# Optimization experiments

Hardware: AMD Instinct MI355X
Metric: run time of the kernel (lower is better)

The kernel has to match this reference:

```python
import jax, jax.numpy as jnp
import numpy as np

EMBED_DIM = 1024
SCALE = float(np.sqrt(EMBED_DIM))


def setup_inputs() -> dict:
    key = jax.random.key(0)
    ks = jax.random.split(key, 4)
    B, S, D = 4, 2048, EMBED_DIM
    x = jax.random.normal(ks[0], (B, S, D), dtype=jnp.float32)
    # causal mask: 1 where attention allowed, 0 where blocked
    mask = jnp.tril(jnp.ones((S, S), dtype=jnp.int32))
    init = 1.0 / np.sqrt(D)
    Wq = jax.random.normal(ks[1], (D, D), dtype=jnp.float32) * init
    Wk = jax.random.normal(ks[2], (D, D), dtype=jnp.float32) * init
    Wv = jax.random.normal(ks[3], (D, D), dtype=jnp.float32) * init
    bq = jnp.zeros((D,), dtype=jnp.float32)
    bk = jnp.zeros((D,), dtype=jnp.float32)
    bv = jnp.zeros((D,), dtype=jnp.float32)
    return {"x": x, "mask": mask, "Wq": Wq, "bq": bq, "Wk": Wk, "bk": bk, "Wv": Wv, "bv": bv}


def reference(x, mask, Wq, bq, Wk, bk, Wv, bv):
    # Q, K, V projections (torch Linear: x @ W^T + b; here W stored as (D_in, D_out))
    q = x @ Wq + bq  # (B, S, D)
    k = x @ Wk + bk
    v = x @ Wv + bv
    # attention scores: Q K^T / sqrt(D)
    scores = jnp.einsum("bsd,btd->bst", q, k) / SCALE  # (B, S, S)
    scores = jnp.where(mask == 0, -jnp.inf, scores)
    attn = jax.nn.softmax(scores, axis=-1)
    # dropout disabled (inference / eval mode)
    out = jnp.einsum("bst,btd->bsd", attn, v)  # (B, S, D)
    return out
```

## Files before the change

### kernel.cpp

```cpp
#include <hip/hip_runtime.h>
#include <math.h>

#define DMODEL 1024
#define SEQ 2048
#define BATCH 4
#define SCALE_INV (1.0f/32.0f)

typedef unsigned short ushort_t;
typedef __attribute__((ext_vector_type(8))) short bf16x8;
typedef __attribute__((ext_vector_type(4))) float f32x4;

__device__ __forceinline__ ushort_t f2bf(float f) {
    unsigned int u = __float_as_uint(f);
    unsigned int rounding = 0x7FFFu + ((u >> 16) & 1u);
    return (ushort_t)((u + rounding) >> 16);
}

#define GLOAD16(SRC, DST) \
    __builtin_amdgcn_global_load_lds( \
        (const __attribute__((address_space(1))) void*)(SRC), \
        (__attribute__((address_space(3))) void*)(DST), 16, 0, 0)

__device__ __forceinline__ int xcd_swz(int bid, int nwg) {
    return (bid & 7) * (nwg >> 3) + (bid >> 3);
}

__device__ __forceinline__ void gemm_core_128(
    const ushort_t* __restrict__ A, int lda,
    const ushort_t* __restrict__ Bt, int ldb,
    int arow0, int brow0, int ksteps,
    ushort_t* As, ushort_t* Bs,
    f32x4 acc[4][4])
{
    const int tid = threadIdx.x;
    const int l   = tid & 63;
    const int w   = tid >> 6;
    const int wr  = w >> 1;
    const int wc  = w & 1;
    const int ke_swz = (((l & 3) ^ ((l >> 2) & 3)) * 8);
    const int kgx = (l >> 4) ^ (l & 3);

    for (int s = 0; s < ksteps; ++s) {
        const int k0 = s * 32;
        #pragma unroll
        for (int i = 0; i < 2; ++i) {
            const int off = i * 4096 + w * 1024 + l * 16;
            const int row = off >> 6;
            GLOAD16(A + (size_t)(arow0 + row) * lda + k0 + ke_swz,
                    (char*)As + i * 4096 + w * 1024);
        }
        #pragma unroll
        for (int i = 0; i < 2; ++i) {
            const int off = i * 4096 + w * 1024 + l * 16;
            const int row = off >> 6;
            GLOAD16(Bt + (size_t)(brow0 + row) * ldb + k0 + ke_swz,
                    (char*)Bs + i * 4096 + w * 1024);
        }
        __syncthreads();

        bf16x8 a[4], b[4];
        #pragma unroll
        for (int m = 0; m < 4; ++m)
            a[m] = *(const bf16x8*)(As + (wr * 64 + m * 16 + (l & 15)) * 32 + kgx * 8);
        #pragma unroll
        for (int n = 0; n < 4; ++n)
            b[n] = *(const bf16x8*)(Bs + (wc * 64 + n * 16 + (l & 15)) * 32 + kgx * 8);
        #pragma unroll
        for (int m = 0; m < 4; ++m)
            #pragma unroll
            for (int n = 0; n < 4; ++n)
                acc[m][n] = __builtin_amdgcn_mfma_f32_16x16x32_bf16(a[m], b[n], acc[m][n], 0, 0, 0);
        __syncthreads();
    }
}

__global__ __launch_bounds__(256) void qkv_gemm_mfma(
    const ushort_t* __restrict__ x,
    const ushort_t* __restrict__ wtq, const ushort_t* __restrict__ wtk, const ushort_t* __restrict__ wtv,
    const float* __restrict__ bq, const float* __restrict__ bk, const float* __restrict__ bv,
    ushort_t* __restrict__ q, ushort_t* __restrict__ k, ushort_t* __restrict__ vt)
{
    __shared__ __align__(16) ushort_t As[128 * 32];
    __shared__ __align__(16) ushort_t Bs[128 * 32];

    const int wg = xcd_swz(blockIdx.x, 8 * 64 * 3);
    const int z  = wg >> 9;
    const int r  = wg & 511;
    const int by = r >> 3;
    const int bx = r & 7;

    const ushort_t* Bt; const float* bias; float scale;
    if (z == 0)      { Bt = wtq; bias = bq; scale = SCALE_INV; }
    else if (z == 1) { Bt = wtk; bias = bk; scale = 1.0f; }
    else             { Bt = wtv; bias = bv; scale = 1.0f; }

    const int arow0 = by * 128;
    const int brow0 = bx * 128;

    f32x4 acc[4][4];
    #pragma unroll
    for (int m = 0; m < 4; ++m)
        #pragma unroll
        for (int n = 0; n < 4; ++n)
            acc[m][n] = (f32x4)(0.f);

    gemm_core_128(x, DMODEL, Bt, DMODEL, arow0, brow0, DMODEL / 32, As, Bs, acc);

    const int l  = threadIdx.x & 63;
    const int w  = threadIdx.x >> 6;
    const int wr = w >> 1, wc = w & 1;

    if (z < 2) {
        ushort_t* out = (z == 0) ? q : k;
        #pragma unroll
        for (int n = 0; n < 4; ++n) {
            const int gcol = brow0 + wc * 64 + n * 16 + (l & 15);
            const float bb = bias[gcol];
            #pragma unroll
            for (int m = 0; m < 4; ++m) {
                #pragma unroll
                for (int j = 0; j < 4; ++j) {
                    const int grow = arow0 + wr * 64 + m * 16 + (l >> 4) * 4 + j;
                    out[(size_t)grow * DMODEL + gcol] = f2bf((acc[m][n][j] + bb) * scale);
                }
            }
        }
    } else {
        ushort_t* vtb = vt + (size_t)(arow0 >> 11) * DMODEL * SEQ;
        #pragma unroll
        for (int n = 0; n < 4; ++n) {
            const int gcol = brow0 + wc * 64 + n * 16 + (l & 15);
            const float bb = bias[gcol];
            #pragma unroll
            for (int m = 0; m < 4; ++m) {
                const int t0 = (arow0 & 2047) + wr * 64 + m * 16 + (l >> 4) * 4;
                ushort4 o;
                o.x = f2bf(acc[m][n][0] + bb);
                o.y = f2bf(acc[m][n][1] + bb);
                o.z = f2bf(acc[m][n][2] + bb);
                o.w = f2bf(acc[m][n][3] + bb);
                *(ushort4*)(vtb + (size_t)gcol * SEQ + t0) = o;
            }
        }
    }
}

__global__ __launch_bounds__(256) void qkt_gemm_mfma(
    const ushort_t* __restrict__ q, const ushort_t* __restrict__ k,
    float* __restrict__ scores)
{
    const int wg = xcd_swz(blockIdx.x, 16 * 16 * BATCH);
    const int b  = wg >> 8;
    const int r  = wg & 255;
    const int st = r >> 4;
    const int tt = r & 15;
    if (tt > st) return;

    __shared__ __align__(16) ushort_t As[128 * 32];
    __shared__ __align__(16) ushort_t Bs[128 * 32];

    const ushort_t* A  = q + (size_t)b * SEQ * DMODEL;
    const ushort_t* Bt = k + (size_t)b * SEQ * DMODEL;
    float* out = scores + (size_t)b * SEQ * SEQ;

    f32x4 acc[4][4];
    #pragma unroll
    for (int m = 0; m < 4; ++m)
        #pragma unroll
        for (int n = 0; n < 4; ++n)
            acc[m][n] = (f32x4)(0.f);

    gemm_core_128(A, DMODEL, Bt, DMODEL, st * 128, tt * 128, DMODEL / 32, As, Bs, acc);

    const int l  = threadIdx.x & 63;
    const int w  = threadIdx.x >> 6;
    const int wr = w >> 1, wc = w & 1;
    #pragma unroll
    for (int m = 0; m < 4; ++m) {
        #pragma unroll
        for (int n = 0; n < 4; ++n) {
            const int gcol = tt * 128 + wc * 64 + n * 16 + (l & 15);
            #pragma unroll
            for (int j = 0; j < 4; ++j) {
                const int grow = st * 128 + wr * 64 + m * 16 + (l >> 4) * 4 + j;
                out[(size_t)grow * SEQ + gcol] = acc[m][n][j];
            }
        }
    }
}

__global__ __launch_bounds__(256) void softmax_rows(float* __restrict__ scores)
{
    const int s = blockIdx.x;
    const int b = blockIdx.y;
    const int tid = threadIdx.x;

    float* row = scores + ((size_t)b * SEQ + s) * SEQ;
    ushort_t* prow = (ushort_t*)row;
    const int nt = s + 1;

    __shared__ float e_sh[SEQ];
    __shared__ float red[256];

    float lmax = -INFINITY;
    const int nt4 = nt >> 2;
    for (int i = tid; i < nt4; i += 256) {
        const float4 f = ((const float4*)row)[i];
        ((float4*)e_sh)[i] = f;
        lmax = fmaxf(lmax, fmaxf(fmaxf(f.x, f.y), fmaxf(f.z, f.w)));
    }
    for (int t = nt4 * 4 + tid; t < nt; t += 256) {
        const float xv = row[t];
        e_sh[t] = xv;
        lmax = fmaxf(lmax, xv);
    }
    red[tid] = lmax;
    __syncthreads();
    for (int off = 128; off > 0; off >>= 1) {
        if (tid < off) red[tid] = fmaxf(red[tid], red[tid + off]);
        __syncthreads();
    }
    const float mx = red[0];
    __syncthreads();

    float lsum = 0.f;
    for (int t = tid; t < nt; t += 256) {
        const float e = __expf(e_sh[t] - mx);
        e_sh[t] = e;
        lsum += e;
    }
    red[tid] = lsum;
    __syncthreads();
    for (int off = 128; off > 0; off >>= 1) {
        if (tid < off) red[tid] += red[tid + off];
        __syncthreads();
    }
    const float inv = 1.0f / red[0];
    __syncthreads();

    const int tmax = ((s >> 7) + 1) << 7;
    for (int t4 = tid * 4; t4 < tmax; t4 += 1024) {
        ushort4 o;
        o.x = (t4     < nt) ? f2bf(e_sh[t4    ] * inv) : (ushort_t)0;
        o.y = (t4 + 1 < nt) ? f2bf(e_sh[t4 + 1] * inv) : (ushort_t)0;
        o.z = (t4 + 2 < nt) ? f2bf(e_sh[t4 + 2] * inv) : (ushort_t)0;
        o.w = (t4 + 3 < nt) ? f2bf(e_sh[t4 + 3] * inv) : (ushort_t)0;
        *(ushort4*)(prow + t4) = o;
    }
}

__global__ __launch_bounds__(256) void pv_gemm_mfma(
    const float* __restrict__ scoresP, const ushort_t* __restrict__ vt,
    float* __restrict__ outp)
{
    const int wg = xcd_swz(blockIdx.x, 8 * 16 * BATCH);
    const int b  = wg >> 7;
    const int r  = wg & 127;
    const int st = r >> 3;
    const int dt = r & 7;

    __shared__ __align__(16) ushort_t As[128 * 32];
    __shared__ __align__(16) ushort_t Bs[128 * 32];

    const ushort_t* A  = (const ushort_t*)(scoresP + (size_t)b * SEQ * SEQ);
    const ushort_t* Bt = vt + (size_t)b * DMODEL * SEQ;
    float* out = outp + (size_t)b * SEQ * DMODEL;

    f32x4 acc[4][4];
    #pragma unroll
    for (int m = 0; m < 4; ++m)
        #pragma unroll
        for (int n = 0; n < 4; ++n)
            acc[m][n] = (f32x4)(0.f);

    const int ksteps = (st + 1) * 4;
    gemm_core_128(A, 2 * SEQ, Bt, SEQ, st * 128, dt * 128, ksteps, As, Bs, acc);

    const int l  = threadIdx.x & 63;
    const int w  = threadIdx.x >> 6;
    const int wr = w >> 1, wc = w & 1;
    #pragma unroll
    for (int m = 0; m < 4; ++m) {
        #pragma unroll
        for (int n = 0; n < 4; ++n) {
            const int gcol = dt * 128 + wc * 64 + n * 16 + (l & 15);
            #pragma unroll
            for (int j = 0; j < 4; ++j) {
                const int grow = st * 128 + wr * 64 + m * 16 + (l >> 4) * 4 + j;
                out[(size_t)grow * DMODEL + gcol] = acc[m][n][j];
            }
        }
    }
}

__global__ __launch_bounds__(256) void convert_bf16(
    const float* __restrict__ in, ushort_t* __restrict__ out, int n4)
{
    const int i = (blockIdx.x * 256 + threadIdx.x);
    if (i < n4) {
        const float4 f = *(const float4*)(in + (size_t)i * 4);
        ushort4 o;
        o.x = f2bf(f.x); o.y = f2bf(f.y); o.z = f2bf(f.z); o.w = f2bf(f.w);
        *(ushort4*)(out + (size_t)i * 4) = o;
    }
}

__global__ __launch_bounds__(256) void transpose_w(
    const float* __restrict__ Wq, const float* __restrict__ Wk, const float* __restrict__ Wv,
    ushort_t* __restrict__ wtq, ushort_t* __restrict__ wtk, ushort_t* __restrict__ wtv)
{
    const float* W; ushort_t* wt;
    const int z = blockIdx.z;
    if (z == 0)      { W = Wq; wt = wtq; }
    else if (z == 1) { W = Wk; wt = wtk; }
    else             { W = Wv; wt = wtv; }

    __shared__ float tile[32][33];
    const int k0 = blockIdx.x * 32, n0 = blockIdx.y * 32;
    const int x = threadIdx.x, y = threadIdx.y;
    #pragma unroll
    for (int i = 0; i < 4; ++i)
        tile[y + i * 8][x] = W[(size_t)(k0 + y + i * 8) * DMODEL + n0 + x];
    __syncthreads();
    #pragma unroll
    for (int i = 0; i < 4; ++i)
        wt[(size_t)(n0 + y + i * 8) * DMODEL + k0 + x] = f2bf(tile[x][y + i * 8]);
}

__global__ __launch_bounds__(1024) void qkv_gemm_f32(
    const float* __restrict__ x,
    const float* __restrict__ Wq, const float* __restrict__ bq,
    const float* __restrict__ Wk, const float* __restrict__ bk,
    const float* __restrict__ Wv, const float* __restrict__ bv,
    float* __restrict__ q, float* __restrict__ k, float* __restrict__ v)
{
    const float* W; const float* bias; float* out;
    const int z = blockIdx.z;
    if (z == 0)      { W = Wq; bias = bq; out = q; }
    else if (z == 1) { W = Wk; bias = bk; out = k; }
    else             { W = Wv; bias = bv; out = v; }

    __shared__ float As[32][33];
    __shared__ float Bs[32][33];
    const int tx = threadIdx.x, ty = threadIdx.y;
    const int row = blockIdx.y * 32 + ty;
    const int col = blockIdx.x * 32 + tx;

    float acc = 0.f;
    for (int k0 = 0; k0 < DMODEL; k0 += 32) {
        As[ty][tx] = x[(size_t)row * DMODEL + k0 + tx];
        Bs[ty][tx] = W[(size_t)(k0 + ty) * DMODEL + col];
        __syncthreads();
        #pragma unroll
        for (int kk = 0; kk < 32; ++kk)
            acc += As[ty][kk] * Bs[kk][tx];
        __syncthreads();
    }
    out[(size_t)row * DMODEL + col] = acc + bias[col];
}

__global__ __launch_bounds__(256) void attn_f32(
    const float* __restrict__ q, const float* __restrict__ k,
    const float* __restrict__ v, float* __restrict__ out)
{
    const int s = blockIdx.x, b = blockIdx.y, tid = threadIdx.x;
    __shared__ float qs[DMODEL];
    __shared__ float sc[SEQ];
    __shared__ float red[256];
    const float* qrow = q + ((size_t)b * SEQ + s) * DMODEL;
    for (int d = tid; d < DMODEL; d += 256) qs[d] = qrow[d];
    __syncthreads();
    const float* kb = k + (size_t)b * SEQ * DMODEL;
    const int nt = s + 1;
    float lmax = -INFINITY;
    for (int t = tid; t < nt; t += 256) {
        const float* krow = kb + (size_t)t * DMODEL;
        float acc = 0.f;
        for (int d = 0; d < DMODEL; d += 4) {
            const float4 kv = *(const float4*)(krow + d);
            acc += qs[d] * kv.x + qs[d+1] * kv.y + qs[d+2] * kv.z + qs[d+3] * kv.w;
        }
        acc *= SCALE_INV; sc[t] = acc; lmax = fmaxf(lmax, acc);
    }
    red[tid] = lmax; __syncthreads();
    for (int off = 128; off > 0; off >>= 1) { if (tid < off) red[tid] = fmaxf(red[tid], red[tid+off]); __syncthreads(); }
    const float mx = red[0]; __syncthreads();
    float lsum = 0.f;
    for (int t = tid; t < nt; t += 256) { const float e = expf(sc[t]-mx); sc[t]=e; lsum+=e; }
    red[tid] = lsum; __syncthreads();
    for (int off = 128; off > 0; off >>= 1) { if (tid < off) red[tid] += red[tid+off]; __syncthreads(); }
    const float inv = 1.0f / red[0]; __syncthreads();
    const float* vb = v + (size_t)b * SEQ * DMODEL;
    float a0=0,a1=0,a2=0,a3=0;
    for (int t = 0; t < nt; ++t) {
        const float p = sc[t];
        const float* vrow = vb + (size_t)t * DMODEL;
        a0 += p*vrow[tid]; a1 += p*vrow[tid+256]; a2 += p*vrow[tid+512]; a3 += p*vrow[tid+768];
    }
    float* orow = out + ((size_t)b * SEQ + s) * DMODEL;
    orow[tid]=a0*inv; orow[tid+256]=a1*inv; orow[tid+512]=a2*inv; orow[tid+768]=a3*inv;
}

extern "C" void kernel_launch(void* const* d_in, const int* in_sizes, int n_in,
                              void* d_out, int out_size, void* d_ws, size_t ws_size,
                              hipStream_t stream)
{
    const float* x  = (const float*)d_in[0];
    const float* Wq = (const float*)d_in[2];
    const float* bq = (const float*)d_in[3];
    const float* Wk = (const float*)d_in[4];
    const float* bk = (const float*)d_in[5];
    const float* Wv = (const float*)d_in[6];
    const float* bv = (const float*)d_in[7];
    float* out = (float*)d_out;

    const size_t SZ_XBF   = (size_t)BATCH * SEQ * DMODEL * 2;
    const size_t SZ_WT    = (size_t)DMODEL * DMODEL * 2;
    const size_t SZ_QKV   = (size_t)BATCH * SEQ * DMODEL * 2;
    const size_t SZ_SC    = (size_t)BATCH * SEQ * SEQ * 4;
    const size_t NEED = SZ_XBF + 3 * SZ_WT + 3 * SZ_QKV + SZ_SC;

    if (ws_size >= NEED) {
        char* p = (char*)d_ws;
        ushort_t* x_bf = (ushort_t*)p;              p += SZ_XBF;
        ushort_t* wtq  = (ushort_t*)p;              p += SZ_WT;
        ushort_t* wtk  = (ushort_t*)p;              p += SZ_WT;
        ushort_t* wtv  = (ushort_t*)p;              p += SZ_WT;
        ushort_t* q_bf = (ushort_t*)p;              p += SZ_QKV;
        ushort_t* k_bf = (ushort_t*)p;              p += SZ_QKV;
        ushort_t* vt   = (ushort_t*)p;              p += SZ_QKV;
        float*    sc   = (float*)p;

        const int n4 = BATCH * SEQ * DMODEL / 4;
        hipLaunchKernelGGL(convert_bf16, dim3((n4 + 255) / 256), dim3(256), 0, stream,
                           x, x_bf, n4);
        hipLaunchKernelGGL(transpose_w, dim3(32, 32, 3), dim3(32, 8), 0, stream,
                           Wq, Wk, Wv, wtq, wtk, wtv);
        hipLaunchKernelGGL(qkv_gemm_mfma, dim3(8 * 64 * 3), dim3(256), 0, stream,
                           x_bf, wtq, wtk, wtv, bq, bk, bv, q_bf, k_bf, vt);
        hipLaunchKernelGGL(qkt_gemm_mfma, dim3(16 * 16 * BATCH), dim3(256), 0, stream,
                           q_bf, k_bf, sc);
        hipLaunchKernelGGL(softmax_rows, dim3(SEQ, BATCH), dim3(256), 0, stream, sc);
        hipLaunchKernelGGL(pv_gemm_mfma, dim3(8 * 16 * BATCH), dim3(256), 0, stream,
                           sc, vt, out);
    } else {
        const size_t elems = (size_t)BATCH * SEQ * DMODEL;
        float* q = (float*)d_ws;
        float* k = q + elems;
        float* v = k + elems;
        hipLaunchKernelGGL(qkv_gemm_f32, dim3(DMODEL / 32, BATCH * SEQ / 32, 3), dim3(32, 32), 0, stream,
                           x, Wq, bq, Wk, bk, Wv, bv, q, k, v);
        hipLaunchKernelGGL(attn_f32, dim3(SEQ, BATCH), dim3(256), 0, stream, q, k, v, out);
    }
}
```

Measured before the change: 206.7 us.

## Merge prep kernels, drop LDS swizzle, widen softmax to 512 threads

Merges the x-to-bf16 conversion and the weight transpose into one prep launch writing a contiguous weight buffer, and simplifies QKV weight selection to pointer arithmetic. Removes the XOR swizzle from the shared GEMM core's LDS load and read addressing, which may bring back LDS bank conflicts. Doubles softmax block size to 512 and vectorises the exp pass with float4. These combine launch-overhead, addressing and softmax parallelism changes with a possible bank-conflict regression.

After: 213.4 us. 3.2% more time.

```diff
diff --git a/kernel.cpp b/kernel.cpp
--- a/kernel.cpp
+++ b/kernel.cpp
@@ -37,8 +37,6 @@
     const int w   = tid >> 6;
     const int wr  = w >> 1;
     const int wc  = w & 1;
-    const int ke_swz = (((l & 3) ^ ((l >> 2) & 3)) * 8);
-    const int kgx = (l >> 4) ^ (l & 3);
 
     for (int s = 0; s < ksteps; ++s) {
         const int k0 = s * 32;
@@ -46,14 +44,16 @@
         for (int i = 0; i < 2; ++i) {
             const int off = i * 4096 + w * 1024 + l * 16;
             const int row = off >> 6;
-            GLOAD16(A + (size_t)(arow0 + row) * lda + k0 + ke_swz,
+            const int ke  = (off & 63) >> 1;
+            GLOAD16(A + (size_t)(arow0 + row) * lda + k0 + ke,
                     (char*)As + i * 4096 + w * 1024);
         }
         #pragma unroll
         for (int i = 0; i < 2; ++i) {
             const int off = i * 4096 + w * 1024 + l * 16;
             const int row = off >> 6;
-            GLOAD16(Bt + (size_t)(brow0 + row) * ldb + k0 + ke_swz,
+            const int ke  = (off & 63) >> 1;
+            GLOAD16(Bt + (size_t)(brow0 + row) * ldb + k0 + ke,
                     (char*)Bs + i * 4096 + w * 1024);
         }
         __syncthreads();
@@ -61,10 +61,10 @@
         bf16x8 a[4], b[4];
         #pragma unroll
         for (int m = 0; m < 4; ++m)
-            a[m] = *(const bf16x8*)(As + (wr * 64 + m * 16 + (l & 15)) * 32 + kgx * 8);
+            a[m] = *(const bf16x8*)(As + (wr * 64 + m * 16 + (l & 15)) * 32 + (l >> 4) * 8);
         #pragma unroll
         for (int n = 0; n < 4; ++n)
-            b[n] = *(const bf16x8*)(Bs + (wc * 64 + n * 16 + (l & 15)) * 32 + kgx * 8);
+            b[n] = *(const bf16x8*)(Bs + (wc * 64 + n * 16 + (l & 15)) * 32 + (l >> 4) * 8);
         #pragma unroll
         for (int m = 0; m < 4; ++m)
             #pragma unroll
@@ -76,7 +76,7 @@
 
 __global__ __launch_bounds__(256) void qkv_gemm_mfma(
     const ushort_t* __restrict__ x,
-    const ushort_t* __restrict__ wtq, const ushort_t* __restrict__ wtk, const ushort_t* __restrict__ wtv,
+    const ushort_t* __restrict__ wt,
     const float* __restrict__ bq, const float* __restrict__ bk, const float* __restrict__ bv,
     ushort_t* __restrict__ q, ushort_t* __restrict__ k, ushort_t* __restrict__ vt)
 {
@@ -89,10 +89,9 @@
     const int by = r >> 3;
     const int bx = r & 7;
 
-    const ushort_t* Bt; const float* bias; float scale;
-    if (z == 0)      { Bt = wtq; bias = bq; scale = SCALE_INV; }
-    else if (z == 1) { Bt = wtk; bias = bk; scale = 1.0f; }
-    else             { Bt = wtv; bias = bv; scale = 1.0f; }
+    const ushort_t* Bt = wt + (size_t)z * DMODEL * DMODEL;
+    const float* bias = (z == 0) ? bq : (z == 1) ? bk : bv;
+    const float scale = (z == 0) ? SCALE_INV : 1.0f;
 
     const int arow0 = by * 128;
     const int brow0 = bx * 128;
@@ -189,7 +188,7 @@
     }
 }
 
-__global__ __launch_bounds__(256) void softmax_rows(float* __restrict__ scores)
+__global__ __launch_bounds__(512) void softmax_rows(float* __restrict__ scores)
 {
     const int s = blockIdx.x;
     const int b = blockIdx.y;
@@ -200,23 +199,23 @@
     const int nt = s + 1;
 
     __shared__ float e_sh[SEQ];
-    __shared__ float red[256];
+    __shared__ float red[512];
 
     float lmax = -INFINITY;
     const int nt4 = nt >> 2;
-    for (int i = tid; i < nt4; i += 256) {
+    for (int i = tid; i < nt4; i += 512) {
         const float4 f = ((const float4*)row)[i];
         ((float4*)e_sh)[i] = f;
         lmax = fmaxf(lmax, fmaxf(fmaxf(f.x, f.y), fmaxf(f.z, f.w)));
     }
-    for (int t = nt4 * 4 + tid; t < nt; t += 256) {
+    for (int t = nt4 * 4 + tid; t < nt; t += 512) {
         const float xv = row[t];
         e_sh[t] = xv;
         lmax = fmaxf(lmax, xv);
     }
     red[tid] = lmax;
     __syncthreads();
-    for (int off = 128; off > 0; off >>= 1) {
+    for (int off = 256; off > 0; off >>= 1) {
         if (tid < off) red[tid] = fmaxf(red[tid], red[tid + off]);
         __syncthreads();
     }
@@ -224,14 +223,21 @@
     __syncthreads();
 
     float lsum = 0.f;
-    for (int t = tid; t < nt; t += 256) {
+    for (int i = tid; i < nt4; i += 512) {
+        float4 f = ((const float4*)e_sh)[i];
+        f.x = __expf(f.x - mx); f.y = __expf(f.y - mx);
+        f.z = __expf(f.z - mx); f.w = __expf(f.w - mx);
+        ((float4*)e_sh)[i] = f;
+        lsum += f.x + f.y + f.z + f.w;
+    }
+    for (int t = nt4 * 4 + tid; t < nt; t += 512) {
         const float e = __expf(e_sh[t] - mx);
         e_sh[t] = e;
         lsum += e;
     }
     red[tid] = lsum;
     __syncthreads();
-    for (int off = 128; off > 0; off >>= 1) {
+    for (int off = 256; off > 0; off >>= 1) {
         if (tid < off) red[tid] += red[tid + off];
         __syncthreads();
     }
@@ -239,7 +245,7 @@
     __syncthreads();
 
     const int tmax = ((s >> 7) + 1) << 7;
-    for (int t4 = tid * 4; t4 < tmax; t4 += 1024) {
+    for (int t4 = tid * 4; t4 < tmax; t4 += 2048) {
         ushort4 o;
         o.x = (t4     < nt) ? f2bf(e_sh[t4    ] * inv) : (ushort_t)0;
         o.y = (t4 + 1 < nt) ? f2bf(e_sh[t4 + 1] * inv) : (ushort_t)0;
@@ -293,38 +299,38 @@
     }
 }
 
-__global__ __launch_bounds__(256) void convert_bf16(
-    const float* __restrict__ in, ushort_t* __restrict__ out, int n4)
-{
-    const int i = (blockIdx.x * 256 + threadIdx.x);
-    if (i < n4) {
-        const float4 f = *(const float4*)(in + (size_t)i * 4);
+__global__ __launch_bounds__(256) void prep_kernel(
+    const float* __restrict__ x, ushort_t* __restrict__ x_bf,
+    const float* __restrict__ Wq, const float* __restrict__ Wk, const float* __restrict__ Wv,
+    ushort_t* __restrict__ wt)
+{
+    __shared__ float tile[32][33];
+    const int bid = blockIdx.x;
+    const int tid = threadIdx.x;
+
+    if (bid < 8192) {
+        const int i = bid * 256 + tid;
+        const float4 f = *(const float4*)(x + (size_t)i * 4);
         ushort4 o;
         o.x = f2bf(f.x); o.y = f2bf(f.y); o.z = f2bf(f.z); o.w = f2bf(f.w);
-        *(ushort4*)(out + (size_t)i * 4) = o;
-    }
-}
-
-__global__ __launch_bounds__(256) void transpose_w(
-    const float* __restrict__ Wq, const float* __restrict__ Wk, const float* __restrict__ Wv,
-    ushort_t* __restrict__ wtq, ushort_t* __restrict__ wtk, ushort_t* __restrict__ wtv)
-{
-    const float* W; ushort_t* wt;
-    const int z = blockIdx.z;
-    if (z == 0)      { W = Wq; wt = wtq; }
-    else if (z == 1) { W = Wk; wt = wtk; }
-    else             { W = Wv; wt = wtv; }
-
-    __shared__ float tile[32][33];
-    const int k0 = blockIdx.x * 32, n0 = blockIdx.y * 32;
-    const int x = threadIdx.x, y = threadIdx.y;
-    #pragma unroll
-    for (int i = 0; i < 4; ++i)
-        tile[y + i * 8][x] = W[(size_t)(k0 + y + i * 8) * DMODEL + n0 + x];
-    __syncthreads();
-    #pragma unroll
-    for (int i = 0; i < 4; ++i)
-        wt[(size_t)(n0 + y + i * 8) * DMODEL + k0 + x] = f2bf(tile[x][y + i * 8]);
+        *(ushort4*)(x_bf + (size_t)i * 4) = o;
+    } else {
+        const int id = bid - 8192;
+        const int z  = id >> 10;
+        const int t  = id & 1023;
+        const int k0 = (t & 31) * 32;
+        const int n0 = (t >> 5) * 32;
+        const float* W = (z == 0) ? Wq : (z == 1) ? Wk : Wv;
+        ushort_t* wtd = wt + (size_t)z * DMODEL * DMODEL;
+        const int x_ = tid & 31, y = tid >> 5;
+        #pragma unroll
+        for (int i = 0; i < 4; ++i)
+            tile[y + i * 8][x_] = W[(size_t)(k0 + y + i * 8) * DMODEL + n0 + x_];
+        __syncthreads();
+        #pragma unroll
+        for (int i = 0; i < 4; ++i)
+            wtd[(size_t)(n0 + y + i * 8) * DMODEL + k0 + x_] = f2bf(tile[x_][y + i * 8]);
+    }
 }
 
 __global__ __launch_bounds__(1024) void qkv_gemm_f32(
@@ -415,32 +421,27 @@
     float* out = (float*)d_out;
 
     const size_t SZ_XBF   = (size_t)BATCH * SEQ * DMODEL * 2;
-    const size_t SZ_WT    = (size_t)DMODEL * DMODEL * 2;
+    const size_t SZ_WT    = 3 * (size_t)DMODEL * DMODEL * 2;
     const size_t SZ_QKV   = (size_t)BATCH * SEQ * DMODEL * 2;
     const size_t SZ_SC    = (size_t)BATCH * SEQ * SEQ * 4;
-    const size_t NEED = SZ_XBF + 3 * SZ_WT + 3 * SZ_QKV + SZ_SC;
+    const size_t NEED = SZ_XBF + SZ_WT + 3 * SZ_QKV + SZ_SC;
 
     if (ws_size >= NEED) {
         char* p = (char*)d_ws;
         ushort_t* x_bf = (ushort_t*)p;              p += SZ_XBF;
-        ushort_t* wtq  = (ushort_t*)p;              p += SZ_WT;
-        ushort_t* wtk  = (ushort_t*)p;              p += SZ_WT;
-        ushort_t* wtv  = (ushort_t*)p;              p += SZ_WT;
+        ushort_t* wt   = (ushort_t*)p;              p += SZ_WT;
         ushort_t* q_bf = (ushort_t*)p;              p += SZ_QKV;
         ushort_t* k_bf = (ushort_t*)p;              p += SZ_QKV;
         ushort_t* vt   = (ushort_t*)p;              p += SZ_QKV;
         float*    sc   = (float*)p;
 
-        const int n4 = BATCH * SEQ * DMODEL / 4;
-        hipLaunchKernelGGL(convert_bf16, dim3((n4 + 255) / 256), dim3(256), 0, stream,
-                           x, x_bf, n4);
-        hipLaunchKernelGGL(transpose_w, dim3(32, 32, 3), dim3(32, 8), 0, stream,
-                           Wq, Wk, Wv, wtq, wtk, wtv);
+        hipLaunchKernelGGL(prep_kernel, dim3(8192 + 3072), dim3(256), 0, stream,
+                           x, x_bf, Wq, Wk, Wv, wt);
         hipLaunchKernelGGL(qkv_gemm_mfma, dim3(8 * 64 * 3), dim3(256), 0, stream,
-                           x_bf, wtq, wtk, wtv, bq, bk, bv, q_bf, k_bf, vt);
+                           x_bf, wt, bq, bk, bv, q_bf, k_bf, vt);
         hipLaunchKernelGGL(qkt_gemm_mfma, dim3(16 * 16 * BATCH), dim3(256), 0, stream,
                            q_bf, k_bf, sc);
-        hipLaunchKernelGGL(softmax_rows, dim3(SEQ, BATCH), dim3(256), 0, stream, sc);
+        hipLaunchKernelGGL(softmax_rows, dim3(SEQ, BATCH), dim3(512), 0, stream, sc);
         hipLaunchKernelGGL(pv_gemm_mfma, dim3(8 * 16 * BATCH), dim3(256), 0, stream,
                            sc, vt, out);
     } else {
```
